# Performance work log

Hardware: AMD Instinct MI355X
Metric: run time of the kernel (lower is better)

Reference implementation:

```python
import jax, jax.numpy as jnp
import numpy as np

EPS = 1e-5  # torch LayerNorm default


def _layer_norm(x, g, b):
    mu = jnp.mean(x, axis=-1, keepdims=True)
    var = jnp.mean(jnp.square(x - mu), axis=-1, keepdims=True)
    return (x - mu) * jax.lax.rsqrt(var + EPS) * g + b


def setup_inputs() -> dict:
    key = jax.random.key(0)
    ks = jax.random.split(key, 8)
    B, S, D = 4, 2048, 1024
    s = 1.0 / np.sqrt(D)
    return {
        "q": jax.random.normal(ks[0], (B, S, D), jnp.float32),
        "k": jax.random.normal(ks[1], (B, S, D), jnp.float32),
        "v": jax.random.normal(ks[2], (B, S, D), jnp.float32),
        "mask": jnp.ones((B, 1, S), jnp.int32),
        "Wq": jax.random.normal(ks[3], (D, D), jnp.float32) * s,
        "Wk": jax.random.normal(ks[4], (D, D), jnp.float32) * s,
        "Wv": jax.random.normal(ks[5], (D, D), jnp.float32) * s,
        "Wo": jax.random.normal(ks[6], (D, D), jnp.float32) * s,
        "ln_q_g": jnp.ones((D,), jnp.float32),
        "ln_q_b": jnp.zeros((D,), jnp.float32),
        "ln_k_g": jnp.ones((D,), jnp.float32),
        "ln_k_b": jnp.zeros((D,), jnp.float32),
        "ln_v_g": jnp.ones((D,), jnp.float32),
        "ln_v_b": jnp.zeros((D,), jnp.float32),
    }


def reference(q, k, v, mask, Wq, Wk, Wv, Wo,
              ln_q_g, ln_q_b, ln_k_g, ln_k_b, ln_v_g, ln_v_b):
    B, Lq, D = q.shape
    H = 16
    dk = D // H
    residual = q
    # pre-LN + bias-free projections
    qh = (_layer_norm(q, ln_q_g, ln_q_b) @ Wq).reshape(B, Lq, H, dk).transpose(0, 2, 1, 3)
    kh = (_layer_norm(k, ln_k_g, ln_k_b) @ Wk).reshape(B, -1, H, dk).transpose(0, 2, 1, 3)
    vh = (_layer_norm(v, ln_v_g, ln_v_b) @ Wv).reshape(B, -1, H, dk).transpose(0, 2, 1, 3)
    # scaled scores [B,H,Lq,Lk]
    scores = jnp.einsum('bhqd,bhkd->bhqk', qh, kh) / jnp.sqrt(jnp.float32(dk))
    pad = (mask == 0)[:, None, :, :]  # [B,1,*,Lk], True where masked
    scores = jnp.where(pad, -jnp.inf, scores)
    attn = jax.nn.softmax(scores, axis=-1)
    attn = jnp.where(pad, 0.0, attn)
    out = jnp.einsum('bhqk,bhkd->bhqd', attn, vh)
    out = out.transpose(0, 2, 1, 3).reshape(B, Lq, D)
    return out @ Wo + residual
```

## Files before the change

### kernel.cpp

```cpp
#include <hip/hip_runtime.h>
#include <stdint.h>

typedef __attribute__((ext_vector_type(8))) short short8;
typedef __attribute__((ext_vector_type(4))) float f32x4;
typedef __attribute__((ext_vector_type(4))) unsigned short us4;

#define B_ 4
#define S_ 2048
#define D_ 1024
#define H_ 16
#define DK_ 64

__device__ __forceinline__ unsigned short f2bf(float f) {
  union { float f; unsigned int u; } c; c.f = f;
  unsigned int r = (c.u + 0x7fffu + ((c.u >> 16) & 1u)) >> 16;
  return (unsigned short)r;
}

__device__ __forceinline__ unsigned int cvt_pk_bf16(float lo, float hi) {
  unsigned int r;
  asm("v_cvt_pk_bf16_f32 %0, %1, %2" : "=v"(r) : "v"(lo), "v"(hi));
  return r;
}

__device__ __forceinline__ float exp2_fast(float x) {
#if __has_builtin(__builtin_amdgcn_exp2f)
  return __builtin_amdgcn_exp2f(x);
#else
  float r; asm("v_exp_f32 %0, %1" : "=v"(r) : "v"(x)); return r;
#endif
}

__device__ __forceinline__ void glds16(const void* g, void* l) {
  __builtin_amdgcn_global_load_lds(
      (__attribute__((address_space(1))) void*)(uintptr_t)g,
      (__attribute__((address_space(3))) void*)l, 16, 0, 0);
}

__device__ __forceinline__ f32x4 mfma_bf16(short8 a, short8 b, f32x4 c) {
  return __builtin_amdgcn_mfma_f32_16x16x32_bf16(a, b, c, 0, 0, 0);
}

__global__ __launch_bounds__(256) void ln_bf16_3(const float* __restrict__ x0,
                                                 const float* __restrict__ x1,
                                                 const float* __restrict__ x2,
                                                 const float* __restrict__ g0,
                                                 const float* __restrict__ g1,
                                                 const float* __restrict__ g2,
                                                 const float* __restrict__ b0,
                                                 const float* __restrict__ b1,
                                                 const float* __restrict__ b2,
                                                 unsigned short* __restrict__ y0,
                                                 unsigned short* __restrict__ y1,
                                                 unsigned short* __restrict__ y2) {
  const int which = blockIdx.y;
  const float* x = which == 0 ? x0 : (which == 1 ? x1 : x2);
  const float* g = which == 0 ? g0 : (which == 1 ? g1 : g2);
  const float* bta = which == 0 ? b0 : (which == 1 ? b1 : b2);
  unsigned short* y = which == 0 ? y0 : (which == 1 ? y1 : y2);

  const int lane = threadIdx.x & 63, wid = threadIdx.x >> 6;
  const int row = blockIdx.x * 4 + wid;
  const float4* xr = (const float4*)(x + (size_t)row * D_);
  float4 v[4];
  float s1 = 0.f, s2 = 0.f;
#pragma unroll
  for (int i = 0; i < 4; ++i) {
    v[i] = xr[i * 64 + lane];
    s1 += v[i].x + v[i].y + v[i].z + v[i].w;
    s2 += v[i].x * v[i].x + v[i].y * v[i].y + v[i].z * v[i].z + v[i].w * v[i].w;
  }
#pragma unroll
  for (int m = 32; m; m >>= 1) { s1 += __shfl_xor(s1, m); s2 += __shfl_xor(s2, m); }
  const float mu = s1 * (1.f / D_);
  const float inv = rsqrtf(s2 * (1.f / D_) - mu * mu + 1e-5f);
  const float4* gp = (const float4*)g;
  const float4* bp = (const float4*)bta;
  us4* yr = (us4*)(y + (size_t)row * D_);
#pragma unroll
  for (int i = 0; i < 4; ++i) {
    float4 gv = gp[i * 64 + lane], bv = bp[i * 64 + lane];
    us4 o;
    o[0] = f2bf((v[i].x - mu) * inv * gv.x + bv.x);
    o[1] = f2bf((v[i].y - mu) * inv * gv.y + bv.y);
    o[2] = f2bf((v[i].z - mu) * inv * gv.z + bv.z);
    o[3] = f2bf((v[i].w - mu) * inv * gv.w + bv.w);
    yr[i * 64 + lane] = o;
  }
}

__global__ void wt_bf16_4(const float* __restrict__ W0, const float* __restrict__ W1,
                          const float* __restrict__ W2, const float* __restrict__ W3,
                          unsigned short* __restrict__ T0, unsigned short* __restrict__ T1,
                          unsigned short* __restrict__ T2, unsigned short* __restrict__ T3) {
  const int which = blockIdx.z;
  const float* W = which == 0 ? W0 : (which == 1 ? W1 : (which == 2 ? W2 : W3));
  unsigned short* Wt = which == 0 ? T0 : (which == 1 ? T1 : (which == 2 ? T2 : T3));
  __shared__ float t[32][33];
  const int n0 = blockIdx.x * 32, k0 = blockIdx.y * 32;
  const int tx = threadIdx.x, ty = threadIdx.y;
  for (int i = ty; i < 32; i += 8) t[i][tx] = W[(size_t)(k0 + i) * D_ + n0 + tx];
  __syncthreads();
  for (int i = ty; i < 32; i += 8)
    Wt[(size_t)(n0 + i) * D_ + k0 + tx] = f2bf(t[tx][i]);
}

__global__ __launch_bounds__(256, 4) void gemm_qkv(const unsigned short* __restrict__ Xq,
                                                   const unsigned short* __restrict__ Xk,
                                                   const unsigned short* __restrict__ Xv,
                                                   const unsigned short* __restrict__ Wq,
                                                   const unsigned short* __restrict__ Wk,
                                                   const unsigned short* __restrict__ Wv,
                                                   unsigned short* __restrict__ Qh,
                                                   unsigned short* __restrict__ Kh,
                                                   unsigned short* __restrict__ Vtb,
                                                   float qscale) {
  constexpr int K = D_;
  constexpr int NT = K / 64;
  __shared__ __attribute__((aligned(16))) unsigned short As[128][64];
  __shared__ __attribute__((aligned(16))) unsigned short Bs[128][64];
  const int z = blockIdx.z;
  const unsigned short* A = z == 0 ? Xq : (z == 1 ? Xk : Xv);
  const unsigned short* Bt = z == 0 ? Wq : (z == 1 ? Wk : Wv);
  const int tid = threadIdx.x;
  const int lane = tid & 63, wid = tid >> 6;
  const int lo16 = lane & 15, hi4 = lane >> 4;
  const int wr = wid >> 1, wc = wid & 1;
  const int gx = (int)gridDim.x;
  const int lid = (int)blockIdx.x + gx * (int)blockIdx.y;
  const int nwg = gx * (int)gridDim.y;
  const int swid = (lid & 7) * (nwg >> 3) + (lid >> 3);
  const int mbase = (swid / gx) * 128, nbase = (swid % gx) * 128;
  const int srow = lane >> 3, scol = (lane & 7) * 8;

  f32x4 acc[4][4] = {};

  for (int kt = 0; kt < NT; ++kt) {
    __syncthreads();
    const int kb = kt * 64;
#pragma unroll
    for (int c = 0; c < 4; ++c) {
      const int ch = wid * 4 + c;
      glds16(A + (size_t)(mbase + ch * 8 + srow) * K + kb + scol,
             (unsigned short*)As + ch * 512);
      glds16(Bt + (size_t)(nbase + ch * 8 + srow) * K + kb + scol,
             (unsigned short*)Bs + ch * 512);
    }
    __syncthreads();
    __builtin_amdgcn_s_setprio(1);
#pragma unroll
    for (int kk = 0; kk < 2; ++kk) {
      short8 af[4], bfr[4];
#pragma unroll
      for (int i = 0; i < 4; ++i)
        af[i] = *(const short8*)(&As[0][0] + (wr * 64 + i * 16 + lo16) * 64 + kk * 32 + hi4 * 8);
#pragma unroll
      for (int j = 0; j < 4; ++j)
        bfr[j] = *(const short8*)(&Bs[0][0] + (wc * 64 + j * 16 + lo16) * 64 + kk * 32 + hi4 * 8);
#pragma unroll
      for (int i = 0; i < 4; ++i)
#pragma unroll
        for (int j = 0; j < 4; ++j) acc[i][j] = mfma_bf16(af[i], bfr[j], acc[i][j]);
    }
    __builtin_amdgcn_s_setprio(0);
  }

  if (z < 2) {
    unsigned short* out = z == 0 ? Qh : Kh;
    const float scale = z == 0 ? qscale : 1.0f;
#pragma unroll
    for (int i = 0; i < 4; ++i) {
      const int row = mbase + wr * 64 + i * 16 + hi4 * 4;
      const int b = row >> 11, s = row & (S_ - 1);
#pragma unroll
      for (int j = 0; j < 4; ++j) {
        const int col = nbase + wc * 64 + j * 16 + lo16;
        const int h = col >> 6, d = col & 63;
        const size_t base = ((size_t)(b * H_ + h) * S_ + s) * DK_ + d;
#pragma unroll
        for (int r = 0; r < 4; ++r) out[base + (size_t)r * DK_] = f2bf(acc[i][j][r] * scale);
      }
    }
  } else {
#pragma unroll
    for (int i = 0; i < 4; ++i) {
      const int row = mbase + wr * 64 + i * 16 + hi4 * 4;
      const int b = row >> 11, s0 = row & (S_ - 1);
#pragma unroll
      for (int j = 0; j < 4; ++j) {
        const int col = nbase + wc * 64 + j * 16 + lo16;
        const int h = col >> 6, d = col & 63;
        us4 w;
#pragma unroll
        for (int r = 0; r < 4; ++r) w[r] = f2bf(acc[i][j][r]);
        *(us4*)(Vtb + ((size_t)(b * H_ + h) * DK_ + d) * S_ + s0) = w;
      }
    }
  }
}

__global__ __launch_bounds__(256, 4) void gemm_out(const unsigned short* __restrict__ A,
                                                   const unsigned short* __restrict__ Bt,
                                                   float* __restrict__ out,
                                                   const float* __restrict__ resid) {
  constexpr int K = D_;
  constexpr int NT = K / 64;
  __shared__ __attribute__((aligned(16))) unsigned short As[128][64];
  __shared__ __attribute__((aligned(16))) unsigned short Bs[128][64];
  const int tid = threadIdx.x;
  const int lane = tid & 63, wid = tid >> 6;
  const int lo16 = lane & 15, hi4 = lane >> 4;
  const int wr = wid >> 1, wc = wid & 1;
  const int gx = (int)gridDim.x;
  const int lid = (int)blockIdx.x + gx * (int)blockIdx.y;
  const int nwg = gx * (int)gridDim.y;
  const int swid = (lid & 7) * (nwg >> 3) + (lid >> 3);
  const int mbase = (swid / gx) * 128, nbase = (swid % gx) * 128;
  const int srow = lane >> 3, scol = (lane & 7) * 8;

  f32x4 acc[4][4] = {};

  for (int kt = 0; kt < NT; ++kt) {
    __syncthreads();
    const int kb = kt * 64;
#pragma unroll
    for (int c = 0; c < 4; ++c) {
      const int ch = wid * 4 + c;
      glds16(A + (size_t)(mbase + ch * 8 + srow) * K + kb + scol,
             (unsigned short*)As + ch * 512);
      glds16(Bt + (size_t)(nbase + ch * 8 + srow) * K + kb + scol,
             (unsigned short*)Bs + ch * 512);
    }
    __syncthreads();
    __builtin_amdgcn_s_setprio(1);
#pragma unroll
    for (int kk = 0; kk < 2; ++kk) {
      short8 af[4], bfr[4];
#pragma unroll
      for (int i = 0; i < 4; ++i)
        af[i] = *(const short8*)(&As[0][0] + (wr * 64 + i * 16 + lo16) * 64 + kk * 32 + hi4 * 8);
#pragma unroll
      for (int j = 0; j < 4; ++j)
        bfr[j] = *(const short8*)(&Bs[0][0] + (wc * 64 + j * 16 + lo16) * 64 + kk * 32 + hi4 * 8);
#pragma unroll
      for (int i = 0; i < 4; ++i)
#pragma unroll
        for (int j = 0; j < 4; ++j) acc[i][j] = mfma_bf16(af[i], bfr[j], acc[i][j]);
    }
    __builtin_amdgcn_s_setprio(0);
  }

#pragma unroll
  for (int i = 0; i < 4; ++i) {
    const int row = mbase + wr * 64 + i * 16 + hi4 * 4;
#pragma unroll
    for (int j = 0; j < 4; ++j) {
      const int col = nbase + wc * 64 + j * 16 + lo16;
      const size_t idx = (size_t)row * D_ + col;
#pragma unroll
      for (int r = 0; r < 4; ++r)
        out[idx + (size_t)r * D_] = acc[i][j][r] + resid[idx + (size_t)r * D_];
    }
  }
}

__global__ __launch_bounds__(512, 2) void attn_k(const unsigned short* __restrict__ Qh,
                                                 const unsigned short* __restrict__ Kh,
                                                 const unsigned short* __restrict__ Vt,
                                                 const int* __restrict__ mask,
                                                 unsigned short* __restrict__ O) {
  __shared__ __attribute__((aligned(16))) unsigned short Ks[2][64][64];
  __shared__ __attribute__((aligned(16))) unsigned short Vs[2][64][64];
  __shared__ __attribute__((aligned(16))) unsigned short Ps[256][64];
  __shared__ int TileOkI[S_ / 64];
  const int tid = threadIdx.x, lane = tid & 63, wid = tid >> 6;
  const int lo16 = lane & 15, hi4 = lane >> 4;
  const int swz = (lo16 & 7) << 3;
  const int lid = (int)blockIdx.x + 8 * (int)blockIdx.y;
  const int swid = (lid & 7) * 64 + (lid >> 3);
  const int qb = swid & 7, bh = swid >> 3;
  const int b = bh >> 4, h = bh & 15;
  const unsigned short* Qb = Qh + (size_t)bh * S_ * DK_;
  const unsigned short* Kb = Kh + (size_t)bh * S_ * DK_;
  const unsigned short* Vb = Vt + (size_t)bh * DK_ * S_;
  const int* mb = mask + b * S_;
  const int srow = lane >> 3;
  const int scolx = ((lane & 7) ^ srow) * 8;

  if (tid < S_ / 64) TileOkI[tid] = 1;
  __syncthreads();
  {
    int okp = 1;
#pragma unroll
    for (int j = 0; j < 4; ++j) okp &= (mb[tid * 4 + j] != 0);
    if (!okp) TileOkI[tid >> 4] = 0;
  }

  short8 qf[2][2];
#pragma unroll
  for (int i = 0; i < 2; ++i)
#pragma unroll
    for (int kk = 0; kk < 2; ++kk)
      qf[i][kk] = *(const short8*)(Qb + (size_t)(qb * 256 + wid * 32 + i * 16 + lo16) * DK_ +
                                   kk * 32 + hi4 * 8);

  f32x4 o[2][4] = {};
  float lsum0 = 0.f, lsum1 = 0.f;

  auto stageKV = [&](int bufi, int kt) {
    glds16(Kb + (size_t)(kt * 64 + wid * 8 + srow) * DK_ + scolx,
           (unsigned short*)&Ks[bufi][0][0] + wid * 512);
    glds16(Vb + (size_t)(wid * 8 + srow) * S_ + kt * 64 + scolx,
           (unsigned short*)&Vs[bufi][0][0] + wid * 512);
  };

  stageKV(0, 0);
  int cur = 0;

  for (int kt = 0; kt < S_ / 64; ++kt) {
    __syncthreads();
    if (kt + 1 < S_ / 64) stageKV(cur ^ 1, kt + 1);

    const unsigned short* Kc = &Ks[cur][0][0];
    const int tok = TileOkI[kt];
    short8 kf[2][4];
#pragma unroll
    for (int kk = 0; kk < 2; ++kk)
#pragma unroll
      for (int nf = 0; nf < 4; ++nf)
        kf[kk][nf] = *(const short8*)(Kc + (nf * 16 + lo16) * 64 + ((kk * 32 + hi4 * 8) ^ swz));
#pragma unroll
    for (int i = 0; i < 2; ++i) {
      f32x4 p[4] = {};
      __builtin_amdgcn_s_setprio(1);
#pragma unroll
      for (int kk = 0; kk < 2; ++kk)
#pragma unroll
        for (int nf = 0; nf < 4; ++nf) p[nf] = mfma_bf16(kf[kk][nf], qf[i][kk], p[nf]);
      __builtin_amdgcn_s_setprio(0);
      if (!tok) {
#pragma unroll
        for (int nf = 0; nf < 4; ++nf)
#pragma unroll
          for (int r = 0; r < 4; ++r)
            if (mb[kt * 64 + nf * 16 + hi4 * 4 + r] == 0) p[nf][r] = -1e30f;
      }
      const int prow = wid * 32 + i * 16 + lo16;
      float ls = 0.f;
#pragma unroll
      for (int nf = 0; nf < 4; ++nf) {
        float e0 = exp2_fast(p[nf][0]);
        float e1 = exp2_fast(p[nf][1]);
        float e2 = exp2_fast(p[nf][2]);
        float e3 = exp2_fast(p[nf][3]);
        ls += (e0 + e1) + (e2 + e3);
        uint2 w;
        w.x = cvt_pk_bf16(e0, e1);
        w.y = cvt_pk_bf16(e2, e3);
        *(uint2*)&Ps[prow][(nf * 16 + hi4 * 4) ^ swz] = w;
      }
      if (i == 0) lsum0 += ls; else lsum1 += ls;
    }
    asm volatile("s_waitcnt lgkmcnt(0)" ::: "memory");
    __builtin_amdgcn_sched_barrier(0);
    const unsigned short* Vc = &Vs[cur][0][0];
    __builtin_amdgcn_s_setprio(1);
#pragma unroll
    for (int kk = 0; kk < 2; ++kk) {
      const int pc = (kk * 32 + hi4 * 8) ^ swz;
      short8 pa0 = *(const short8*)((const unsigned short*)Ps + (wid * 32 + 0 + lo16) * 64 + pc);
      short8 pa1 = *(const short8*)((const unsigned short*)Ps + (wid * 32 + 16 + lo16) * 64 + pc);
#pragma unroll
      for (int df = 0; df < 4; ++df) {
        short8 vf = *(const short8*)(Vc + (df * 16 + lo16) * 64 + pc);
        o[0][df] = mfma_bf16(pa0, vf, o[0][df]);
        o[1][df] = mfma_bf16(pa1, vf, o[1][df]);
      }
    }
    __builtin_amdgcn_s_setprio(0);
    cur ^= 1;
  }

  lsum0 += __shfl_xor(lsum0, 16); lsum0 += __shfl_xor(lsum0, 32);
  lsum1 += __shfl_xor(lsum1, 16); lsum1 += __shfl_xor(lsum1, 32);
#pragma unroll
  for (int i = 0; i < 2; ++i) {
#pragma unroll
    for (int r = 0; r < 4; ++r) {
      const int ql = hi4 * 4 + r;
      const float l = __shfl(i == 0 ? lsum0 : lsum1, ql);
      const float rl = l > 0.f ? 1.f / l : 0.f;
      const int srowg = qb * 256 + wid * 32 + i * 16 + ql;
      const size_t base = ((size_t)b * S_ + srowg) * D_ + h * 64;
#pragma unroll
      for (int df = 0; df < 4; ++df) O[base + df * 16 + lo16] = f2bf(o[i][df][r] * rl);
    }
  }
}

extern "C" void kernel_launch(void* const* d_in, const int* in_sizes, int n_in,
                              void* d_out, int out_size, void* d_ws, size_t ws_size,
                              hipStream_t stream) {
  const float* q = (const float*)d_in[0];
  const float* k = (const float*)d_in[1];
  const float* v = (const float*)d_in[2];
  const int* mask = (const int*)d_in[3];
  const float* Wq = (const float*)d_in[4];
  const float* Wk = (const float*)d_in[5];
  const float* Wv = (const float*)d_in[6];
  const float* Wo = (const float*)d_in[7];
  const float* lnqg = (const float*)d_in[8];
  const float* lnqb = (const float*)d_in[9];
  const float* lnkg = (const float*)d_in[10];
  const float* lnkb = (const float*)d_in[11];
  const float* lnvg = (const float*)d_in[12];
  const float* lnvb = (const float*)d_in[13];

  uint8_t* ws = (uint8_t*)d_ws;
  const size_t MB = 1024ull * 1024ull;
  unsigned short* Xq = (unsigned short*)(ws + 0 * MB);
  unsigned short* Xk = (unsigned short*)(ws + 16 * MB);
  unsigned short* Xv = (unsigned short*)(ws + 32 * MB);
  unsigned short* Wqt = (unsigned short*)(ws + 48 * MB);
  unsigned short* Wkt = (unsigned short*)(ws + 50 * MB);
  unsigned short* Wvt = (unsigned short*)(ws + 52 * MB);
  unsigned short* Wot = (unsigned short*)(ws + 54 * MB);
  unsigned short* Qh = (unsigned short*)(ws + 56 * MB);
  unsigned short* Kh = (unsigned short*)(ws + 72 * MB);
  unsigned short* Vtb = Xq;
  unsigned short* Ob = Xk;

  hipLaunchKernelGGL(wt_bf16_4, dim3(32, 32, 4), dim3(32, 8), 0, stream,
                     Wq, Wk, Wv, Wo, Wqt, Wkt, Wvt, Wot);

  hipLaunchKernelGGL(ln_bf16_3, dim3(2048, 3), dim3(256), 0, stream,
                     q, k, v, lnqg, lnkg, lnvg, lnqb, lnkb, lnvb, Xq, Xk, Xv);

  const float qscale = 0.125f * 1.4426950408889634f;
  hipLaunchKernelGGL(gemm_qkv, dim3(D_ / 128, (B_ * S_) / 128, 3), dim3(256), 0, stream,
                     Xq, Xk, Xv, Wqt, Wkt, Wvt, Qh, Kh, Vtb, qscale);

  hipLaunchKernelGGL(attn_k, dim3(S_ / 256, B_ * H_), dim3(512), 0, stream, Qh, Kh, Vtb, mask, Ob);

  hipLaunchKernelGGL(gemm_out, dim3(D_ / 128, (B_ * S_) / 128), dim3(256), 0, stream,
                     Ob, Wot, (float*)d_out, q);
}
```

Before: 202.2 us.

## Single-buffer attention K/V tiles and raise occupancy, compute tile mask via ballot

Drops the double-buffered K/V LDS staging in the attention kernel in favour of single buffers, with a barrier after each load, and raises the launch-bounds occupancy hint from 2 to 6 blocks. The shared per-tile mask array is replaced by a per-wave bitmask built with __all over the mask row. The aim is to shrink LDS use and register pressure so more waves are resident and hide latency, replacing explicit prefetch. The cost is that each tile load is now exposed behind two barriers, and tighter register limits may cause spills.

Result: slower. 701.8 us (+247.2%).

```diff
diff --git a/kernel.cpp b/kernel.cpp
--- a/kernel.cpp
+++ b/kernel.cpp
@@ -264,15 +264,14 @@
   }
 }
 
-__global__ __launch_bounds__(512, 2) void attn_k(const unsigned short* __restrict__ Qh,
+__global__ __launch_bounds__(512, 6) void attn_k(const unsigned short* __restrict__ Qh,
                                                  const unsigned short* __restrict__ Kh,
                                                  const unsigned short* __restrict__ Vt,
                                                  const int* __restrict__ mask,
                                                  unsigned short* __restrict__ O) {
-  __shared__ __attribute__((aligned(16))) unsigned short Ks[2][64][64];
-  __shared__ __attribute__((aligned(16))) unsigned short Vs[2][64][64];
+  __shared__ __attribute__((aligned(16))) unsigned short Ks[64][64];
+  __shared__ __attribute__((aligned(16))) unsigned short Vs[64][64];
   __shared__ __attribute__((aligned(16))) unsigned short Ps[256][64];
-  __shared__ int TileOkI[S_ / 64];
   const int tid = threadIdx.x, lane = tid & 63, wid = tid >> 6;
   const int lo16 = lane & 15, hi4 = lane >> 4;
   const int swz = (lo16 & 7) << 3;
@@ -287,14 +286,10 @@
   const int srow = lane >> 3;
   const int scolx = ((lane & 7) ^ srow) * 8;
 
-  if (tid < S_ / 64) TileOkI[tid] = 1;
-  __syncthreads();
-  {
-    int okp = 1;
-#pragma unroll
-    for (int j = 0; j < 4; ++j) okp &= (mb[tid * 4 + j] != 0);
-    if (!okp) TileOkI[tid >> 4] = 0;
-  }
+  unsigned int tmask = 0u;
+#pragma unroll
+  for (int j = 0; j < S_ / 64; ++j)
+    tmask |= (__all(mb[j * 64 + lane] != 0) ? 1u : 0u) << j;
 
   short8 qf[2][2];
 #pragma unroll
@@ -307,28 +302,21 @@
   f32x4 o[2][4] = {};
   float lsum0 = 0.f, lsum1 = 0.f;
 
-  auto stageKV = [&](int bufi, int kt) {
+  for (int kt = 0; kt < S_ / 64; ++kt) {
+    __syncthreads();
     glds16(Kb + (size_t)(kt * 64 + wid * 8 + srow) * DK_ + scolx,
-           (unsigned short*)&Ks[bufi][0][0] + wid * 512);
+           (unsigned short*)&Ks[0][0] + wid * 512);
     glds16(Vb + (size_t)(wid * 8 + srow) * S_ + kt * 64 + scolx,
-           (unsigned short*)&Vs[bufi][0][0] + wid * 512);
-  };
-
-  stageKV(0, 0);
-  int cur = 0;
-
-  for (int kt = 0; kt < S_ / 64; ++kt) {
-    __syncthreads();
-    if (kt + 1 < S_ / 64) stageKV(cur ^ 1, kt + 1);
-
-    const unsigned short* Kc = &Ks[cur][0][0];
-    const int tok = TileOkI[kt];
+           (unsigned short*)&Vs[0][0] + wid * 512);
+    __syncthreads();
+
+    const int tok = (tmask >> kt) & 1;
     short8 kf[2][4];
 #pragma unroll
     for (int kk = 0; kk < 2; ++kk)
 #pragma unroll
       for (int nf = 0; nf < 4; ++nf)
-        kf[kk][nf] = *(const short8*)(Kc + (nf * 16 + lo16) * 64 + ((kk * 32 + hi4 * 8) ^ swz));
+        kf[kk][nf] = *(const short8*)(&Ks[0][0] + (nf * 16 + lo16) * 64 + ((kk * 32 + hi4 * 8) ^ swz));
 #pragma unroll
     for (int i = 0; i < 2; ++i) {
       f32x4 p[4] = {};
@@ -363,7 +351,6 @@
     }
     asm volatile("s_waitcnt lgkmcnt(0)" ::: "memory");
     __builtin_amdgcn_sched_barrier(0);
-    const unsigned short* Vc = &Vs[cur][0][0];
     __builtin_amdgcn_s_setprio(1);
 #pragma unroll
     for (int kk = 0; kk < 2; ++kk) {
@@ -372,13 +359,12 @@
       short8 pa1 = *(const short8*)((const unsigned short*)Ps + (wid * 32 + 16 + lo16) * 64 + pc);
 #pragma unroll
       for (int df = 0; df < 4; ++df) {
-        short8 vf = *(const short8*)(Vc + (df * 16 + lo16) * 64 + pc);
+        short8 vf = *(const short8*)(&Vs[0][0] + (df * 16 + lo16) * 64 + pc);
         o[0][df] = mfma_bf16(pa0, vf, o[0][df]);
         o[1][df] = mfma_bf16(pa1, vf, o[1][df]);
       }
     }
     __builtin_amdgcn_s_setprio(0);
-    cur ^= 1;
   }
 
   lsum0 += __shfl_xor(lsum0, 16); lsum0 += __shfl_xor(lsum0, 32);
```
